# Kernel optimization log

Measured on AMD Instinct MI355X. Metric: run time of the kernel, lower is better.

The kernel has to match this reference:

```python
import jax, jax.numpy as jnp
import numpy as np
from jax import lax

EPS = 1e-12

def _ln(x, bias):
    # zero_mean=False, scale=False LayerNorm: RMS-style normalize + bias
    var = jnp.mean(x * x, axis=-1, keepdims=True)
    return x / jnp.sqrt(var + EPS) + bias

def _lru(h, nu_log, theta_log, b_re, b_im, c_re, c_im, d):
    # h: [B,S,H]; diagonal complex linear recurrence (LRU)
    lam = jnp.exp(-jnp.exp(nu_log) + 1j * jnp.exp(theta_log))  # [U] complex
    gamma = jnp.sqrt(jnp.clip(1.0 - jnp.abs(lam) ** 2, 0.0, None)).astype(h.dtype)  # [U]
    Bu = (jnp.einsum('bsh,uh->bsu', h, b_re) + 1j * jnp.einsum('bsh,uh->bsu', h, b_im)) * gamma  # [B,S,U]
    a = jnp.broadcast_to(lam, Bu.shape)
    def binop(e1, e2):
        a1, x1 = e1
        a2, x2 = e2
        return a1 * a2, a2 * x1 + x2
    _, states = lax.associative_scan(binop, (a, Bu), axis=1)  # [B,S,U] complex
    y = (jnp.einsum('bsu,hu->bsh', jnp.real(states), c_re)
         - jnp.einsum('bsu,hu->bsh', jnp.imag(states), c_im))
    return y + d * h

def setup_inputs() -> dict:
    key = jax.random.key(0)
    ks = jax.random.split(key, 12)
    B, S, H, L, F, V, P = 4, 2048, 1024, 4, 4096, 32000, 2048
    s = 0.02
    return {
        'input_ids': jax.random.randint(ks[0], (B, S), 0, V),
        'word_emb': jax.random.normal(ks[1], (V, H), jnp.float32) * s,
        'pos_emb': jax.random.normal(ks[2], (P, H), jnp.float32) * s,
        'nu_log': jax.random.normal(ks[3], (L, H), jnp.float32) * 0.5,
        'theta_log': jax.random.normal(ks[4], (L, H), jnp.float32) * 0.5,
        'B_re': jax.random.normal(ks[5], (L, H, H), jnp.float32) / np.sqrt(H),
        'B_im': jax.random.normal(ks[6], (L, H, H), jnp.float32) / np.sqrt(H),
        'C_re': jax.random.normal(ks[7], (L, H, H), jnp.float32) / np.sqrt(H),
        'C_im': jax.random.normal(ks[8], (L, H, H), jnp.float32) / np.sqrt(H),
        'D': jax.random.normal(ks[9], (L, H), jnp.float32),
        'rnn_norm_bias': jnp.zeros((L, H), jnp.float32),
        'w1': jax.random.normal(ks[10], (L, F, H), jnp.float32) * s,
        'b1': jnp.zeros((L, F), jnp.float32),
        'w2': jax.random.normal(ks[11], (L, H, F), jnp.float32) * s,
        'b2': jnp.zeros((L, H), jnp.float32),
        'ffn_norm_bias': jnp.zeros((L, H), jnp.float32),
    }

def reference(input_ids, word_emb, pos_emb, nu_log, theta_log, B_re, B_im,
              C_re, C_im, D, rnn_norm_bias, w1, b1, w2, b2, ffn_norm_bias):
    S = input_ids.shape[1]
    pos_ids = jnp.arange(S)
    h = word_emb[input_ids] + pos_emb[pos_ids][None, :, :]  # [B,S,H]
    L = nu_log.shape[0]
    for l in range(L):
        rnn_out = _lru(h, nu_log[l], theta_log[l], B_re[l], B_im[l], C_re[l], C_im[l], D[l])
        h = _ln(h + rnn_out, rnn_norm_bias[l])
        ffn = jnp.einsum('bsf,hf->bsh',
                         jax.nn.gelu(jnp.einsum('bsh,fh->bsf', h, w1[l]) + b1[l], approximate=False),
                         w2[l]) + b2[l]
        h = _ln(h + ffn, ffn_norm_bias[l])
    return h
```

## Files before the change

### kernel.cpp

```cpp
#include <hip/hip_runtime.h>
#include <hip/hip_bf16.h>
#include <math.h>

typedef __attribute__((ext_vector_type(8))) short short8;
typedef __attribute__((ext_vector_type(4))) float f32x4;

__device__ __forceinline__ float bf2f(unsigned short u) {
  union { unsigned int i; float f; } v; v.i = ((unsigned int)u) << 16; return v.f;
}
__device__ __forceinline__ unsigned short f2bf(float f) {
  union { float f; unsigned int i; } v; v.f = f;
  unsigned int r = v.i + 0x7fffu + ((v.i >> 16) & 1u);
  return (unsigned short)(r >> 16);
}
__device__ __forceinline__ uint4 cvt8(const float* __restrict__ src, float scale) {
  float4 a = *(const float4*)src;
  float4 b = *(const float4*)(src + 4);
  uint4 o; unsigned short* op = (unsigned short*)&o;
  op[0] = f2bf(a.x * scale); op[1] = f2bf(a.y * scale);
  op[2] = f2bf(a.z * scale); op[3] = f2bf(a.w * scale);
  op[4] = f2bf(b.x * scale); op[5] = f2bf(b.y * scale);
  op[6] = f2bf(b.z * scale); op[7] = f2bf(b.w * scale);
  return o;
}
__device__ __forceinline__ void glds16(const unsigned short* g, unsigned short* s) {
  __builtin_amdgcn_global_load_lds(
      (const __attribute__((address_space(1))) unsigned int*)g,
      (__attribute__((address_space(3))) unsigned int*)s, 16, 0, 0);
}

__global__ void embed_k(const int* __restrict__ ids, const float* __restrict__ we,
                        const float* __restrict__ pe, unsigned short* __restrict__ h) {
  int t = blockIdx.x * 256 + threadIdx.x;
  int c8 = (t & 127) * 8, row = t >> 7;
  int s = row & 2047;
  int id = ids[row];
  const float* ap = we + (size_t)id * 1024 + c8;
  const float* bp = pe + (size_t)s * 1024 + c8;
  float4 a0 = *(const float4*)ap, a1 = *(const float4*)(ap + 4);
  float4 b0 = *(const float4*)bp, b1 = *(const float4*)(bp + 4);
  uint4 o; unsigned short* op = (unsigned short*)&o;
  op[0] = f2bf(a0.x + b0.x); op[1] = f2bf(a0.y + b0.y);
  op[2] = f2bf(a0.z + b0.z); op[3] = f2bf(a0.w + b0.w);
  op[4] = f2bf(a1.x + b1.x); op[5] = f2bf(a1.y + b1.y);
  op[6] = f2bf(a1.z + b1.z); op[7] = f2bf(a1.w + b1.w);
  *(uint4*)(h + (size_t)row * 1024 + c8) = o;
}

__global__ void prep_lam_k(const float* __restrict__ nu_log,
                           const float* __restrict__ theta_log,
                           float* __restrict__ lamP) {
  int t = blockIdx.x * 256 + threadIdx.x;
  float nu = nu_log[t], th = theta_log[t];
  float mag = expf(-expf(nu));
  float eth = expf(th);
  float lr = mag * cosf(eth), li = mag * sinf(eth);
  float g2 = 1.0f - mag * mag; if (g2 < 0.f) g2 = 0.f;
  float pr = 1.f, pi = 0.f;
#pragma unroll 1
  for (int i = 0; i < 64; ++i) { float nr = pr * lr - pi * li; pi = pr * li + pi * lr; pr = nr; }
  lamP[t] = lr;
  lamP[4096 + t] = li;
  lamP[2 * 4096 + t] = sqrtf(g2);
  lamP[3 * 4096 + t] = pr;
  lamP[4 * 4096 + t] = pi;
}

__global__ void prep_w_k(const float* __restrict__ Bre, const float* __restrict__ Bim,
                         const float* __restrict__ Cre, const float* __restrict__ Cim,
                         const float* __restrict__ gamma, unsigned short* __restrict__ Bw,
                         unsigned short* __restrict__ Cw) {
  int t = blockIdx.x * 256 + threadIdx.x;
  if (t < 262144) {
    int n = t >> 7, h8 = (t & 127) * 8;
    int u = n & 1023;
    const float* src = (n < 1024 ? Bre : Bim) + (size_t)u * 1024 + h8;
    *(uint4*)(Bw + (size_t)n * 1024 + h8) = cvt8(src, gamma[u]);
  } else {
    int t2 = t - 262144;
    int hrow = t2 >> 8, u8 = (t2 & 255) * 8;
    uint4 o;
    if (u8 < 1024) o = cvt8(Cre + (size_t)hrow * 1024 + u8, 1.0f);
    else           o = cvt8(Cim + (size_t)hrow * 1024 + (u8 - 1024), -1.0f);
    *(uint4*)(Cw + (size_t)hrow * 2048 + u8) = o;
  }
}

__global__ void prep_ffn_k(const float* __restrict__ w1l, const float* __restrict__ w2l,
                           unsigned short* __restrict__ w1c, unsigned short* __restrict__ w2c,
                           int c) {
  int t = blockIdx.x * 256 + threadIdx.x;
  if (t < 131072) {
    size_t off = (size_t)t * 8;
    *(uint4*)(w1c + off) = cvt8(w1l + (size_t)c * 1024 * 1024 + off, 1.0f);
  } else {
    int t2 = t - 131072;
    int n = t2 >> 7, k8 = (t2 & 127) * 8;
    *(uint4*)(w2c + (size_t)n * 1024 + k8) =
        cvt8(w2l + (size_t)n * 4096 + (size_t)c * 1024 + k8, 1.0f);
  }
}

template <int EPI>
__global__ __launch_bounds__(256, 2) void gemm_nt(
    const unsigned short* __restrict__ A, const unsigned short* __restrict__ Bm,
    void* __restrict__ Cout, const float* __restrict__ bias, int M, int N, int K) {
  __shared__ unsigned short As[128 * 32];
  __shared__ unsigned short Bs[128 * 32];
  const int tid = threadIdx.x;
  const int lane = tid & 63;
  const int wave = tid >> 6;
  const int quad = lane >> 4, r = lane & 15;
  const int wm = (wave >> 1) * 64, wn = (wave & 1) * 64;
  const size_t row0 = (size_t)blockIdx.x * 128;
  const size_t col0 = (size_t)blockIdx.y * 128;
  const unsigned short* Ab = A + row0 * K;
  const unsigned short* Bb = Bm + col0 * K;
  const int li0 = tid, li1 = 256 + tid;
  const int rw0 = li0 >> 2, sg0 = (li0 & 3) * 8;
  const int rw1 = li1 >> 2, sg1 = (li1 & 3) * 8;
  unsigned short* As0 = As + wave * 512;
  unsigned short* Bs0 = Bs + wave * 512;
  unsigned short* As1 = As + 2048 + wave * 512;
  unsigned short* Bs1 = Bs + 2048 + wave * 512;
  const unsigned short* Ap0 = Ab + (size_t)rw0 * K + sg0;
  const unsigned short* Bp0 = Bb + (size_t)rw0 * K + sg0;
  const unsigned short* Ap1 = Ab + (size_t)rw1 * K + sg1;
  const unsigned short* Bp1 = Bb + (size_t)rw1 * K + sg1;

  f32x4 acc[4][4];
#pragma unroll
  for (int i = 0; i < 4; ++i)
#pragma unroll
    for (int j = 0; j < 4; ++j) acc[i][j] = (f32x4){0.f, 0.f, 0.f, 0.f};

  for (int k0 = 0; k0 < K; k0 += 32) {
    __syncthreads();
    glds16(Ap0 + k0, As0);
    glds16(Bp0 + k0, Bs0);
    glds16(Ap1 + k0, As1);
    glds16(Bp1 + k0, Bs1);
    __syncthreads();
    short8 aF[4], bF[4];
#pragma unroll
    for (int i = 0; i < 4; ++i) aF[i] = *(const short8*)(As + (wm + i * 16 + r) * 32 + quad * 8);
#pragma unroll
    for (int j = 0; j < 4; ++j) bF[j] = *(const short8*)(Bs + (wn + j * 16 + r) * 32 + quad * 8);
#pragma unroll
    for (int i = 0; i < 4; ++i)
#pragma unroll
      for (int j = 0; j < 4; ++j)
        acc[i][j] = __builtin_amdgcn_mfma_f32_16x16x32_bf16(aF[i], bF[j], acc[i][j], 0, 0, 0);
  }
  unsigned short* Cb = (unsigned short*)Cout;
  float* Cf = (float*)Cout;
#pragma unroll
  for (int j = 0; j < 4; ++j) {
    const size_t gcol = col0 + wn + j * 16 + r;
    float bv = 0.f;
    if (EPI == 2 || EPI == 3) bv = bias[gcol];
#pragma unroll
    for (int i = 0; i < 4; ++i) {
      const size_t grow = row0 + wm + i * 16 + quad * 4;
#pragma unroll
      for (int tt = 0; tt < 4; ++tt) {
        float v = acc[i][j][tt] + bv;
        size_t idx = (grow + tt) * (size_t)N + gcol;
        if (EPI == 2) {
          v = 0.5f * v * (1.0f + erff(v * 0.70710678118654752f));
          Cb[idx] = f2bf(v);
        } else if (EPI == 0) {
          Cb[idx] = f2bf(v);
        } else if (EPI == 3) {
          Cf[idx] = v;
        } else {
          Cf[idx] += v;
        }
      }
    }
  }
}

__global__ void scan_carry_k(const unsigned short* __restrict__ Bu, const float* __restrict__ lamP,
                             float* __restrict__ carry, int l) {
  int t = blockIdx.x * 256 + threadIdx.x;
  int u = t & 1023, c = (t >> 10) & 31, b = t >> 15;
  float lr = lamP[l * 1024 + u], li = lamP[4096 + l * 1024 + u];
  const unsigned short* base = Bu + ((size_t)(b * 2048 + c * 64)) * 2048 + u;
  float sr = 0.f, si = 0.f;
  for (int g = 0; g < 4; ++g) {
#pragma unroll
    for (int j = 0; j < 16; ++j) {
      size_t off = (size_t)(g * 16 + j) * 2048;
      float vr = bf2f(base[off]), vi = bf2f(base[off + 1024]);
      float nr = lr * sr - li * si + vr;
      si = lr * si + li * sr + vi;
      sr = nr;
    }
  }
  size_t idx = ((size_t)b * 32 + c) * 1024 + u;
  carry[idx] = sr; carry[131072 + idx] = si;
}

__global__ void scan_comb_k(const float* __restrict__ carry, const float* __restrict__ lamP,
                            float* __restrict__ inst, int l) {
  int t = blockIdx.x * 256 + threadIdx.x;
  int u = t & 1023, b = t >> 10;
  float tr = lamP[3 * 4096 + l * 1024 + u], ti = lamP[4 * 4096 + l * 1024 + u];
  float pr = 0.f, pi = 0.f;
  for (int c = 0; c < 32; ++c) {
    size_t idx = ((size_t)b * 32 + c) * 1024 + u;
    inst[idx] = pr; inst[131072 + idx] = pi;
    float cr = carry[idx], ci = carry[131072 + idx];
    float nr = tr * pr - ti * pi + cr;
    pi = tr * pi + ti * pr + ci;
    pr = nr;
  }
}

__global__ void scan_final_k(unsigned short* __restrict__ Bu, const float* __restrict__ lamP,
                             const float* __restrict__ inst, int l) {
  int t = blockIdx.x * 256 + threadIdx.x;
  int u = t & 1023, c = (t >> 10) & 31, b = t >> 15;
  float lr = lamP[l * 1024 + u], li = lamP[4096 + l * 1024 + u];
  size_t idx = ((size_t)b * 32 + c) * 1024 + u;
  float sr = inst[idx], si = inst[131072 + idx];
  unsigned short* base = Bu + ((size_t)(b * 2048 + c * 64)) * 2048 + u;
  for (int g = 0; g < 4; ++g) {
#pragma unroll
    for (int j = 0; j < 16; ++j) {
      size_t off = (size_t)(g * 16 + j) * 2048;
      float vr = bf2f(base[off]), vi = bf2f(base[off + 1024]);
      float nr = lr * sr - li * si + vr;
      si = lr * si + li * sr + vi;
      sr = nr;
      base[off] = f2bf(sr); base[off + 1024] = f2bf(si);
    }
  }
}

template <int HASD, int YF32, int OUTF32>
__global__ void ln_k(const unsigned short* __restrict__ h, const void* __restrict__ yv,
                     const float* __restrict__ Dv, const float* __restrict__ bias,
                     void* __restrict__ outv) {
  int wave = threadIdx.x >> 6, lane = threadIdx.x & 63;
  size_t row = (size_t)blockIdx.x * 4 + wave;
  const unsigned short* hr = h + row * 1024;
  float x[16]; float ss = 0.f;
#pragma unroll
  for (int cc = 0; cc < 2; ++cc) {
    int col = cc * 512 + lane * 8;
    uint4 hv = *(const uint4*)(hr + col);
    const unsigned short* hp = (const unsigned short*)&hv;
    float yf[8];
    if (YF32) {
      const float* yr = (const float*)yv + row * 1024 + col;
      float4 y0 = *(const float4*)yr, y1 = *(const float4*)(yr + 4);
      yf[0] = y0.x; yf[1] = y0.y; yf[2] = y0.z; yf[3] = y0.w;
      yf[4] = y1.x; yf[5] = y1.y; yf[6] = y1.z; yf[7] = y1.w;
    } else {
      uint4 yv4 = *(const uint4*)((const unsigned short*)yv + row * 1024 + col);
      const unsigned short* yp = (const unsigned short*)&yv4;
#pragma unroll
      for (int j = 0; j < 8; ++j) yf[j] = bf2f(yp[j]);
    }
    if (HASD) {
      const float* dp = Dv + col;
      float4 d0 = *(const float4*)dp, d1 = *(const float4*)(dp + 4);
      float df[8] = {d0.x, d0.y, d0.z, d0.w, d1.x, d1.y, d1.z, d1.w};
#pragma unroll
      for (int j = 0; j < 8; ++j) {
        float hf = bf2f(hp[j]);
        float v = hf + yf[j] + df[j] * hf;
        x[cc * 8 + j] = v; ss += v * v;
      }
    } else {
#pragma unroll
      for (int j = 0; j < 8; ++j) {
        float v = bf2f(hp[j]) + yf[j];
        x[cc * 8 + j] = v; ss += v * v;
      }
    }
  }
#pragma unroll
  for (int off = 32; off > 0; off >>= 1) ss += __shfl_xor(ss, off);
  float rs = rsqrtf(ss * (1.0f / 1024.0f) + 1e-12f);
#pragma unroll
  for (int cc = 0; cc < 2; ++cc) {
    int col = cc * 512 + lane * 8;
    const float* bp = bias + col;
    float4 b0 = *(const float4*)bp, b1 = *(const float4*)(bp + 4);
    float bf[8] = {b0.x, b0.y, b0.z, b0.w, b1.x, b1.y, b1.z, b1.w};
    if (OUTF32) {
      float* op = (float*)outv + row * 1024 + col;
      float4 o0, o1;
      o0.x = x[cc*8+0]*rs + bf[0]; o0.y = x[cc*8+1]*rs + bf[1];
      o0.z = x[cc*8+2]*rs + bf[2]; o0.w = x[cc*8+3]*rs + bf[3];
      o1.x = x[cc*8+4]*rs + bf[4]; o1.y = x[cc*8+5]*rs + bf[5];
      o1.z = x[cc*8+6]*rs + bf[6]; o1.w = x[cc*8+7]*rs + bf[7];
      *(float4*)op = o0; *(float4*)(op + 4) = o1;
    } else {
      uint4 o; unsigned short* op = (unsigned short*)&o;
#pragma unroll
      for (int j = 0; j < 8; ++j) op[j] = f2bf(x[cc * 8 + j] * rs + bf[j]);
      *(uint4*)((unsigned short*)outv + row * 1024 + col) = o;
    }
  }
}

extern "C" void kernel_launch(void* const* d_in, const int* in_sizes, int n_in,
                              void* d_out, int out_size, void* d_ws, size_t ws_size,
                              hipStream_t stream) {
  const int H = 1024, F = 4096;
  const int*   ids = (const int*)d_in[0];
  const float* we  = (const float*)d_in[1];
  const float* pe  = (const float*)d_in[2];
  const float* nu  = (const float*)d_in[3];
  const float* th  = (const float*)d_in[4];
  const float* Bre = (const float*)d_in[5];
  const float* Bim = (const float*)d_in[6];
  const float* Cre = (const float*)d_in[7];
  const float* Cim = (const float*)d_in[8];
  const float* Dv  = (const float*)d_in[9];
  const float* rnb = (const float*)d_in[10];
  const float* w1  = (const float*)d_in[11];
  const float* b1  = (const float*)d_in[12];
  const float* w2  = (const float*)d_in[13];
  const float* b2  = (const float*)d_in[14];
  const float* fnb = (const float*)d_in[15];
  float* out = (float*)d_out;

  char* w = (char*)d_ws;
  float* lamP  = (float*)w; w += (size_t)5 * 4096 * 4;
  float* carry = (float*)w; w += (size_t)2 * 131072 * 4;
  float* inst  = (float*)w; w += (size_t)2 * 131072 * 4;
  unsigned short* Bw   = (unsigned short*)w; w += (size_t)2048 * 1024 * 2;
  unsigned short* Cw   = (unsigned short*)w; w += (size_t)1024 * 2048 * 2;
  unsigned short* w1c  = (unsigned short*)w; w += (size_t)1024 * 1024 * 2;
  unsigned short* w2c  = (unsigned short*)w; w += (size_t)1024 * 1024 * 2;
  unsigned short* hcur = (unsigned short*)w; w += (size_t)8192 * 1024 * 2;
  unsigned short* Bu   = (unsigned short*)w;
  float*          facc = (float*)Bu;
  w += (size_t)8192 * 2048 * 2;
  unsigned short* ybt  = (unsigned short*)w; w += (size_t)8192 * 1024 * 2;

  embed_k<<<4096, 256, 0, stream>>>(ids, we, pe, hcur);
  prep_lam_k<<<16, 256, 0, stream>>>(nu, th, lamP);

  for (int l = 0; l < 4; ++l) {
    prep_w_k<<<2048, 256, 0, stream>>>(Bre + (size_t)l * H * H, Bim + (size_t)l * H * H,
                                       Cre + (size_t)l * H * H, Cim + (size_t)l * H * H,
                                       lamP + 2 * 4096 + l * 1024, Bw, Cw);
    gemm_nt<0><<<dim3(64, 16), 256, 0, stream>>>(hcur, Bw, Bu, nullptr, 8192, 2048, 1024);
    scan_carry_k<<<512, 256, 0, stream>>>(Bu, lamP, carry, l);
    scan_comb_k<<<16, 256, 0, stream>>>(carry, lamP, inst, l);
    scan_final_k<<<512, 256, 0, stream>>>(Bu, lamP, inst, l);
    gemm_nt<0><<<dim3(64, 8), 256, 0, stream>>>(Bu, Cw, ybt, nullptr, 8192, 1024, 2048);
    ln_k<1, 0, 0><<<2048, 256, 0, stream>>>(hcur, ybt, Dv + l * H, rnb + l * H, hcur);
    for (int c = 0; c < 4; ++c) {
      prep_ffn_k<<<1024, 256, 0, stream>>>(w1 + (size_t)l * F * H, w2 + (size_t)l * H * F,
                                           w1c, w2c, c);
      gemm_nt<2><<<dim3(64, 8), 256, 0, stream>>>(hcur, w1c, ybt,
                                                  b1 + (size_t)l * F + c * 1024, 8192, 1024, 1024);
      if (c == 0)
        gemm_nt<3><<<dim3(64, 8), 256, 0, stream>>>(ybt, w2c, facc, b2 + (size_t)l * H,
                                                    8192, 1024, 1024);
      else
        gemm_nt<4><<<dim3(64, 8), 256, 0, stream>>>(ybt, w2c, facc, nullptr,
                                                    8192, 1024, 1024);
    }
    if (l == 3)
      ln_k<0, 1, 1><<<2048, 256, 0, stream>>>(hcur, facc, nullptr, fnb + l * H, out);
    else
      ln_k<0, 1, 0><<<2048, 256, 0, stream>>>(hcur, facc, nullptr, fnb + l * H, hcur);
  }
}
```

Measured before the change: 2.004 ms.

## Double-buffer GEMM LDS tiles and run FFN as two full-width GEMMs

The GEMM main loop now uses two LDS buffers, issuing the global-to-LDS loads for the next K-tile before computing on the current one, so each iteration needs one barrier instead of two. The FFN no longer loops over four 1024-wide chunks with read-modify-write accumulation into an fp32 buffer. It converts the full w1/w2 once per layer, runs a single 8192x4096 GEMM with the GELU epilogue into a new 64MB bf16 intermediate, then one K=4096 GEMM. This cuts launches and accumulator traffic at the cost of more workspace and doubled LDS per block, which may lower occupancy.

```diff
diff --git a/kernel.cpp b/kernel.cpp
--- a/kernel.cpp
+++ b/kernel.cpp
@@ -87,17 +87,14 @@
 }
 
 __global__ void prep_ffn_k(const float* __restrict__ w1l, const float* __restrict__ w2l,
-                           unsigned short* __restrict__ w1c, unsigned short* __restrict__ w2c,
-                           int c) {
-  int t = blockIdx.x * 256 + threadIdx.x;
-  if (t < 131072) {
-    size_t off = (size_t)t * 8;
-    *(uint4*)(w1c + off) = cvt8(w1l + (size_t)c * 1024 * 1024 + off, 1.0f);
+                           unsigned short* __restrict__ w1b, unsigned short* __restrict__ w2b) {
+  int t = blockIdx.x * 256 + threadIdx.x;
+  size_t off = (size_t)t * 8;
+  if (t < 524288) {
+    *(uint4*)(w1b + off) = cvt8(w1l + off, 1.0f);
   } else {
-    int t2 = t - 131072;
-    int n = t2 >> 7, k8 = (t2 & 127) * 8;
-    *(uint4*)(w2c + (size_t)n * 1024 + k8) =
-        cvt8(w2l + (size_t)n * 4096 + (size_t)c * 1024 + k8, 1.0f);
+    size_t o2 = off - 4194304;
+    *(uint4*)(w2b + o2) = cvt8(w2l + o2, 1.0f);
   }
 }
 
@@ -105,8 +102,8 @@
 __global__ __launch_bounds__(256, 2) void gemm_nt(
     const unsigned short* __restrict__ A, const unsigned short* __restrict__ Bm,
     void* __restrict__ Cout, const float* __restrict__ bias, int M, int N, int K) {
-  __shared__ unsigned short As[128 * 32];
-  __shared__ unsigned short Bs[128 * 32];
+  __shared__ unsigned short As[2 * 128 * 32];
+  __shared__ unsigned short Bs[2 * 128 * 32];
   const int tid = threadIdx.x;
   const int lane = tid & 63;
   const int wave = tid >> 6;
@@ -134,23 +131,37 @@
 #pragma unroll
     for (int j = 0; j < 4; ++j) acc[i][j] = (f32x4){0.f, 0.f, 0.f, 0.f};
 
-  for (int k0 = 0; k0 < K; k0 += 32) {
-    __syncthreads();
-    glds16(Ap0 + k0, As0);
-    glds16(Bp0 + k0, Bs0);
-    glds16(Ap1 + k0, As1);
-    glds16(Bp1 + k0, Bs1);
-    __syncthreads();
+  glds16(Ap0, As0);
+  glds16(Bp0, Bs0);
+  glds16(Ap1, As1);
+  glds16(Bp1, Bs1);
+  __syncthreads();
+
+  const int nk = K >> 5;
+  int cur = 0;
+  for (int t = 0; t < nk; ++t) {
+    if (t + 1 < nk) {
+      const int kn = (t + 1) << 5;
+      const int nb = (cur ^ 1) * 4096;
+      glds16(Ap0 + kn, As0 + nb);
+      glds16(Bp0 + kn, Bs0 + nb);
+      glds16(Ap1 + kn, As1 + nb);
+      glds16(Bp1 + kn, Bs1 + nb);
+    }
+    const unsigned short* Ac = As + cur * 4096;
+    const unsigned short* Bc = Bs + cur * 4096;
     short8 aF[4], bF[4];
 #pragma unroll
-    for (int i = 0; i < 4; ++i) aF[i] = *(const short8*)(As + (wm + i * 16 + r) * 32 + quad * 8);
-#pragma unroll
-    for (int j = 0; j < 4; ++j) bF[j] = *(const short8*)(Bs + (wn + j * 16 + r) * 32 + quad * 8);
+    for (int i = 0; i < 4; ++i) aF[i] = *(const short8*)(Ac + (wm + i * 16 + r) * 32 + quad * 8);
+#pragma unroll
+    for (int j = 0; j < 4; ++j) bF[j] = *(const short8*)(Bc + (wn + j * 16 + r) * 32 + quad * 8);
 #pragma unroll
     for (int i = 0; i < 4; ++i)
 #pragma unroll
       for (int j = 0; j < 4; ++j)
         acc[i][j] = __builtin_amdgcn_mfma_f32_16x16x32_bf16(aF[i], bF[j], acc[i][j], 0, 0, 0);
+    __syncthreads();
+    cur ^= 1;
   }
   unsigned short* Cb = (unsigned short*)Cout;
   float* Cf = (float*)Cout;
@@ -171,10 +182,8 @@
           Cb[idx] = f2bf(v);
         } else if (EPI == 0) {
           Cb[idx] = f2bf(v);
-        } else if (EPI == 3) {
+        } else {
           Cf[idx] = v;
-        } else {
-          Cf[idx] += v;
         }
       }
     }
@@ -336,13 +345,14 @@
   float* inst  = (float*)w; w += (size_t)2 * 131072 * 4;
   unsigned short* Bw   = (unsigned short*)w; w += (size_t)2048 * 1024 * 2;
   unsigned short* Cw   = (unsigned short*)w; w += (size_t)1024 * 2048 * 2;
-  unsigned short* w1c  = (unsigned short*)w; w += (size_t)1024 * 1024 * 2;
-  unsigned short* w2c  = (unsigned short*)w; w += (size_t)1024 * 1024 * 2;
+  unsigned short* w1b  = (unsigned short*)w; w += (size_t)4096 * 1024 * 2;
+  unsigned short* w2b  = (unsigned short*)w; w += (size_t)1024 * 4096 * 2;
   unsigned short* hcur = (unsigned short*)w; w += (size_t)8192 * 1024 * 2;
   unsigned short* Bu   = (unsigned short*)w;
   float*          facc = (float*)Bu;
   w += (size_t)8192 * 2048 * 2;
   unsigned short* ybt  = (unsigned short*)w; w += (size_t)8192 * 1024 * 2;
+  unsigned short* t1   = (unsigned short*)w; w += (size_t)8192 * 4096 * 2;
 
   embed_k<<<4096, 256, 0, stream>>>(ids, we, pe, hcur);
   prep_lam_k<<<16, 256, 0, stream>>>(nu, th, lamP);
@@ -357,18 +367,12 @@
     scan_final_k<<<512, 256, 0, stream>>>(Bu, lamP, inst, l);
     gemm_nt<0><<<dim3(64, 8), 256, 0, stream>>>(Bu, Cw, ybt, nullptr, 8192, 1024, 2048);
     ln_k<1, 0, 0><<<2048, 256, 0, stream>>>(hcur, ybt, Dv + l * H, rnb + l * H, hcur);
-    for (int c = 0; c < 4; ++c) {
-      prep_ffn_k<<<1024, 256, 0, stream>>>(w1 + (size_t)l * F * H, w2 + (size_t)l * H * F,
-                                           w1c, w2c, c);
-      gemm_nt<2><<<dim3(64, 8), 256, 0, stream>>>(hcur, w1c, ybt,
-                                                  b1 + (size_t)l * F + c * 1024, 8192, 1024, 1024);
-      if (c == 0)
-        gemm_nt<3><<<dim3(64, 8), 256, 0, stream>>>(ybt, w2c, facc, b2 + (size_t)l * H,
-                                                    8192, 1024, 1024);
-      else
-        gemm_nt<4><<<dim3(64, 8), 256, 0, stream>>>(ybt, w2c, facc, nullptr,
-                                                    8192, 1024, 1024);
-    }
+    prep_ffn_k<<<4096, 256, 0, stream>>>(w1 + (size_t)l * F * H, w2 + (size_t)l * H * F,
+                                         w1b, w2b);
+    gemm_nt<2><<<dim3(64, 32), 256, 0, stream>>>(hcur, w1b, t1,
+                                                 b1 + (size_t)l * F, 8192, 4096, 1024);
+    gemm_nt<3><<<dim3(64, 8), 256, 0, stream>>>(t1, w2b, facc, b2 + (size_t)l * H,
+                                                8192, 1024, 4096);
     if (l == 3)
       ln_k<0, 1, 1><<<2048, 256, 0, stream>>>(hcur, facc, nullptr, fnb + l * H, out);
     else
```

New measurement: 1.667 ms. 1.2x faster.
